# Kernel optimization log

Measured on AMD Instinct MI355X. Metric: run time of the kernel, lower is better.

The kernel has to match this reference:

```python
import jax, jax.numpy as jnp
import numpy as np

B, C, H, W = 32, 3, 224, 224
HID, EM, NCLS = 128, 64, 10


def _mlp(x, w1, b1, w2, b2):
    return jax.nn.relu(x @ w1 + b1) @ w2 + b2


def _grid(h, w):
    # generate_grid_coords(h, w, (-10,10), (-10,10)) -> [h*w, 2], row-major over (y, x)
    ys = jnp.linspace(-10.0, 10.0, h)
    xs = jnp.linspace(-10.0, 10.0, w)
    gy, gx = jnp.meshgrid(ys, xs, indexing='ij')
    return jnp.stack([gy.ravel(), gx.ravel()], axis=-1)


def setup_inputs() -> dict:
    key = jax.random.key(0)
    ks = jax.random.split(key, 16)
    def lin(k, fi, fo):
        return (jax.random.normal(k, (fi, fo), jnp.float32) / np.sqrt(fi)).astype(jnp.float32)
    inp = {"images": jax.random.normal(ks[0], (B, C, H, W), dtype=jnp.float32)}
    specs = [("obs", C, EM), ("loc", 2, EM), ("ol", 2 * EM, EM), ("cls", EM, NCLS)]
    i = 1
    for n, fi, fo in specs:
        inp[f"w_{n}1"] = lin(ks[i], fi, HID); i += 1
        inp[f"b_{n}1"] = jnp.zeros((HID,), jnp.float32)
        inp[f"w_{n}2"] = lin(ks[i], HID, fo); i += 1
        inp[f"b_{n}2"] = jnp.zeros((fo,), jnp.float32)
    return inp


def reference(images, w_obs1, b_obs1, w_obs2, b_obs2,
              w_loc1, b_loc1, w_loc2, b_loc2,
              w_ol1, b_ol1, w_ol2, b_ol2,
              w_cls1, b_cls1, w_cls2, b_cls2):
    b, c, h, w = images.shape
    n = h * w
    # to_set_representation: [B,C,H,W] -> [B, N, C]
    obss = images.reshape(b, c, n).transpose(0, 2, 1)
    locs = _grid(h, w)                                       # [N, 2]
    em_loc = _mlp(locs, w_loc1, b_loc1, w_loc2, b_loc2)       # [N, EM] (shared, tiled over batch)
    em_obs = _mlp(obss, w_obs1, b_obs1, w_obs2, b_obs2)       # [B, N, EM]
    em = jnp.concatenate(
        [em_obs, jnp.broadcast_to(em_loc[None], (b, n, em_loc.shape[-1]))], axis=-1)
    em_obsloc = _mlp(em, w_ol1, b_ol1, w_ol2, b_ol2)          # [B, N, EM]
    em_obsloc = jax.nn.softplus(em_obsloc)                    # non_negative=True
    em_set = em_obsloc.sum(axis=1)                            # sum-pool over set dim
    logits = _mlp(em_set, w_cls1, b_cls1, w_cls2, b_cls2)     # [B, NCLS]
    return logits
```

## Files before the change

kernel.cpp:

```cpp
#include <hip/hip_runtime.h>

#define N_PIX 50176
#define W_IMG 224
#define ROWS 32
#define NBX 24

typedef __attribute__((ext_vector_type(8))) short s8v;
typedef __attribute__((ext_vector_type(4))) float f4v;
typedef __attribute__((ext_vector_type(2))) __bf16 bf2v;

__device__ __forceinline__ unsigned short f2bf(float f) {
    __bf16 h = (__bf16)f;
    return __builtin_bit_cast(unsigned short, h);
}
__device__ __forceinline__ unsigned int pack2bf(float lo, float hi) {
    bf2v v = {(__bf16)lo, (__bf16)hi};
    return __builtin_bit_cast(unsigned int, v);
}

#define SWZ(r, cb)  (((r) << 8) + ((cb) ^ (((r) & 15) << 4)))
#define CSWZ(r, cb) (((r) << 7) + ((cb) ^ (((r) & 7) << 4)))

__device__ __forceinline__ void gld_lds16(const void* g, void* l) {
    __builtin_amdgcn_global_load_lds(
        (const __attribute__((address_space(1))) unsigned int*)g,
        (__attribute__((address_space(3))) unsigned int*)l, 16, 0, 0);
}

__global__ void k0_weights(const float* __restrict__ w_obs2, const float* __restrict__ b_obs2,
                           const float* __restrict__ w_ol1, const float* __restrict__ b_ol1,
                           const float* __restrict__ w_ol2, const float* __restrict__ w_loc2,
                           unsigned short* __restrict__ Wk,
                           unsigned short* __restrict__ wol2t,
                           unsigned short* __restrict__ wloc2t,
                           float* __restrict__ bias_c) {
    int bid = blockIdx.x, t = threadIdx.x;
    if (bid < 64) {
        int lin = bid * 256 + t;
        int n = lin >> 7, k = lin & 127;
        float s = 0.f;
        #pragma unroll
        for (int e = 0; e < 64; ++e) s = fmaf(w_obs2[k * 64 + e], w_ol1[e * 128 + n], s);
        Wk[n * 192 + k] = f2bf(s);
    } else if (bid < 96) {
        int lin = (bid - 64) * 256 + t;
        int n = lin >> 6, k = lin & 63;
        Wk[n * 192 + 128 + k] = f2bf(w_ol1[(64 + k) * 128 + n]);
    } else if (bid < 128) {
        int lin = (bid - 96) * 256 + t;
        int n = lin >> 7, k = lin & 127;
        wol2t[n * 128 + k] = f2bf(w_ol2[k * 64 + n]);
    } else if (bid < 160) {
        int lin = (bid - 128) * 256 + t;
        int n = lin >> 7, k = lin & 127;
        wloc2t[n * 128 + k] = f2bf(w_loc2[k * 64 + n]);
    } else {
        if (t < 128) {
            float s = b_ol1[t];
            #pragma unroll
            for (int e = 0; e < 64; ++e) s = fmaf(b_obs2[e], w_ol1[e * 128 + t], s);
            bias_c[t] = s;
        }
    }
}

__global__ __launch_bounds__(256) void k1_loc(
        const float* __restrict__ w_loc1, const float* __restrict__ b_loc1,
        const unsigned short* __restrict__ wloc2t, const float* __restrict__ b_loc2,
        unsigned short* __restrict__ emloc) {
    __shared__ char hbuf[64 * 256];
    typedef __attribute__((ext_vector_type(4))) unsigned int u4v;

    const int t = threadIdx.x;
    const int n0 = blockIdx.x * 64;
    const int row = t >> 2, h0 = (t & 3) * 32;
    {
        int n = n0 + row;
        int iy = n / W_IMG, ix = n % W_IMG;
        float y = -10.f + (20.f / 223.f) * (float)iy;
        float x = -10.f + (20.f / 223.f) * (float)ix;
        #pragma unroll
        for (int q4 = 0; q4 < 4; ++q4) {
            int hb = h0 + q4 * 8;
            u4v pk;
            #pragma unroll
            for (int jj = 0; jj < 2; ++jj) {
                f4v wy = *(const f4v*)(w_loc1 + hb + jj * 4);
                f4v wx = *(const f4v*)(w_loc1 + 128 + hb + jj * 4);
                f4v bb = *(const f4v*)(b_loc1 + hb + jj * 4);
                #pragma unroll
                for (int j2 = 0; j2 < 2; ++j2) {
                    float v0 = fmaxf(fmaf(y, wy[j2 * 2], fmaf(x, wx[j2 * 2], bb[j2 * 2])), 0.f);
                    float v1 = fmaxf(fmaf(y, wy[j2 * 2 + 1], fmaf(x, wx[j2 * 2 + 1], bb[j2 * 2 + 1])), 0.f);
                    pk[jj * 2 + j2] = pack2bf(v0, v1);
                }
            }
            *(u4v*)(hbuf + SWZ(row, hb * 2)) = pk;
        }
    }
    __syncthreads();
    {
        const int w = t >> 6, l = t & 63;
        const int l15 = l & 15, lg = l >> 4;
        s8v a[4];
        #pragma unroll
        for (int ks = 0; ks < 4; ++ks)
            a[ks] = *(const s8v*)(hbuf + SWZ(w * 16 + l15, ks * 64 + lg * 16));
        #pragma unroll
        for (int nt = 0; nt < 4; ++nt) {
            f4v acc = {0.f, 0.f, 0.f, 0.f};
            #pragma unroll
            for (int ks = 0; ks < 4; ++ks) {
                s8v bfr = *(const s8v*)(wloc2t + (nt * 16 + l15) * 128 + ks * 32 + lg * 8);
                acc = __builtin_amdgcn_mfma_f32_16x16x32_bf16(a[ks], bfr, acc, 0, 0, 0);
            }
            float bb = b_loc2[nt * 16 + l15];
            int o = nt * 16 + l15;
            #pragma unroll
            for (int r = 0; r < 4; ++r) {
                int n = n0 + w * 16 + lg * 4 + r;
                emloc[(size_t)n * 64 + (o ^ ((n & 7) << 3))] = f2bf(acc[r] + bb);
            }
        }
    }
}

__global__ __launch_bounds__(256, 2) void k2_main(
        const float* __restrict__ images,
        const float* __restrict__ w_obs1, const float* __restrict__ b_obs1,
        const unsigned short* __restrict__ Wk, const float* __restrict__ biasc,
        const unsigned short* __restrict__ wol2t, const float* __restrict__ b_ol2,
        const unsigned short* __restrict__ emloc,
        float* __restrict__ part)
{
    __shared__ char bufA[2][ROWS * 256];
    __shared__ char bufB[2][ROWS * 256];
    __shared__ char bufC[2][ROWS * 128];
    __shared__ f4v bufI4[2][24];
    __shared__ float red[4][16];

    const int t = threadIdx.x;
    const int w = t >> 6, l = t & 63;
    const int l15 = l & 15, lg = l >> 4;
    const int cq = w;
    const int bx = blockIdx.x, b = blockIdx.y;
    const int start = bx * 65 + (bx < 8 ? bx : 8);
    const int cnt = 65 + (bx < 8 ? 1 : 0);
    const size_t imgb = (size_t)b * 3 * N_PIX;
    #define PBASE(k) ((start + (k)) * ROWS)

    s8v a1[2];
    #pragma unroll
    for (int mt = 0; mt < 2; ++mt) {
        int hh = cq * 32 + mt * 16 + l15;
        unsigned int lo = pack2bf(w_obs1[hh], w_obs1[128 + hh]);
        unsigned int hi = pack2bf(w_obs1[256 + hh], b_obs1[hh]);
        if (lg != 0) { lo = 0u; hi = 0u; }
        typedef __attribute__((ext_vector_type(4))) unsigned int u4;
        u4 u = {lo, hi, 0u, 0u};
        a1[mt] = __builtin_bit_cast(s8v, u);
    }

    s8v bw[2][6];
    #pragma unroll
    for (int nt = 0; nt < 2; ++nt) {
        int col = cq * 32 + nt * 16 + l15;
        #pragma unroll
        for (int ks = 0; ks < 6; ++ks)
            bw[nt][ks] = *(const s8v*)(Wk + col * 192 + ks * 32 + lg * 8);
    }
    s8v w2f[4];
    {
        int o = cq * 16 + l15;
        #pragma unroll
        for (int ks = 0; ks < 4; ++ks)
            w2f[ks] = *(const s8v*)(wol2t + o * 128 + ks * 32 + lg * 8);
    }
    const f4v bias30 = *(const f4v*)(biasc + cq * 32 + lg * 4);
    const f4v bias31 = *(const f4v*)(biasc + cq * 32 + 16 + lg * 4);
    const f4v bias4  = *(const f4v*)(b_ol2 + cq * 16 + lg * 4);

    f4v spacc = {0.f, 0.f, 0.f, 0.f};

    if (w == 1 && l < 24) {
        const char* src = (const char*)(images + imgb + (l >> 3) * N_PIX + PBASE(0)) + (l & 7) * 16;
        gld_lds16(src, (char*)bufI4[0]);
    }
    __syncthreads();

    for (int i = 0; i <= cnt + 1; ++i) {
        const int par = i & 1;
        if (i < cnt) {
            const char* src = (const char*)emloc +
                (size_t)(PBASE(i) + w * 8 + (l >> 3)) * 128 + (l & 7) * 16;
            gld_lds16(src, (char*)bufC[par] + w * 1024);
        }
        if (i + 1 < cnt && w == 1 && l < 24) {
            const char* src = (const char*)(images + imgb + (l >> 3) * N_PIX +
                                            PBASE(i + 1)) + (l & 7) * 16;
            gld_lds16(src, (char*)bufI4[par ^ 1]);
        }
        if (i < cnt) {
            const float* bI = (const float*)bufI4[par];
            char* bA = bufA[par];
            #pragma unroll
            for (int nt2 = 0; nt2 < 2; ++nt2) {
                const int p = nt2 * 16 + l15;
                float x0 = bI[p], x1 = bI[32 + p], x2 = bI[64 + p];
                typedef __attribute__((ext_vector_type(4))) unsigned int u4;
                u4 u = {pack2bf(x0, x1), pack2bf(x2, 1.0f), 0u, 0u};
                s8v bfr = __builtin_bit_cast(s8v, u);
                #pragma unroll
                for (int mt = 0; mt < 2; ++mt) {
                    f4v acc = {0.f, 0.f, 0.f, 0.f};
                    acc = __builtin_amdgcn_mfma_f32_16x16x32_bf16(a1[mt], bfr, acc, 0, 0, 0);
                    f4v z = {0.f, 0.f, 0.f, 0.f};
                    acc = __builtin_elementwise_max(acc, z);
                    uint2 pk;
                    pk.x = pack2bf(acc[0], acc[1]);
                    pk.y = pack2bf(acc[2], acc[3]);
                    *(uint2*)(bA + SWZ(p, cq * 64 + mt * 32 + lg * 8)) = pk;
                }
            }
        }
        if (i >= 1 && i <= cnt) {
            const char* bA = bufA[par ^ 1];
            const char* bC = bufC[par ^ 1];
            char* bB = bufB[par ^ 1];
            #pragma unroll
            for (int ms = 0; ms < 2; ++ms) {
                const int p = ms * 16 + l15;
                s8v bf[4];
                #pragma unroll
                for (int ks = 0; ks < 4; ++ks)
                    bf[ks] = *(const s8v*)(bA + SWZ(p, ks * 64 + lg * 16));
                s8v c0 = *(const s8v*)(bC + CSWZ(p, lg * 16));
                s8v c1 = *(const s8v*)(bC + CSWZ(p, lg * 16 + 64));
                f4v acc0 = {0.f, 0.f, 0.f, 0.f}, acc1 = {0.f, 0.f, 0.f, 0.f};
                __builtin_amdgcn_s_setprio(1);
                #pragma unroll
                for (int ks = 0; ks < 4; ++ks) {
                    acc0 = __builtin_amdgcn_mfma_f32_16x16x32_bf16(bw[0][ks], bf[ks], acc0, 0, 0, 0);
                    acc1 = __builtin_amdgcn_mfma_f32_16x16x32_bf16(bw[1][ks], bf[ks], acc1, 0, 0, 0);
                }
                acc0 = __builtin_amdgcn_mfma_f32_16x16x32_bf16(bw[0][4], c0, acc0, 0, 0, 0);
                acc1 = __builtin_amdgcn_mfma_f32_16x16x32_bf16(bw[1][4], c0, acc1, 0, 0, 0);
                acc0 = __builtin_amdgcn_mfma_f32_16x16x32_bf16(bw[0][5], c1, acc0, 0, 0, 0);
                acc1 = __builtin_amdgcn_mfma_f32_16x16x32_bf16(bw[1][5], c1, acc1, 0, 0, 0);
                __builtin_amdgcn_s_setprio(0);
                f4v v0 = acc0 + bias30, v1 = acc1 + bias31;
                f4v z = {0.f, 0.f, 0.f, 0.f};
                v0 = __builtin_elementwise_max(v0, z);
                v1 = __builtin_elementwise_max(v1, z);
                uint2 w0p, w1p;
                w0p.x = pack2bf(v0[0], v0[1]);
                w0p.y = pack2bf(v0[2], v0[3]);
                w1p.x = pack2bf(v1[0], v1[1]);
                w1p.y = pack2bf(v1[2], v1[3]);
                *(uint2*)(bB + SWZ(p, cq * 64 + lg * 8)) = w0p;
                *(uint2*)(bB + SWZ(p, cq * 64 + 32 + lg * 8)) = w1p;
            }
        }
        if (i >= 2) {
            const char* bB = bufB[par];
            #pragma unroll
            for (int ms = 0; ms < 2; ++ms) {
                const int p = ms * 16 + l15;
                s8v bf[4];
                #pragma unroll
                for (int ks = 0; ks < 4; ++ks)
                    bf[ks] = *(const s8v*)(bB + SWZ(p, ks * 64 + lg * 16));
                f4v acc = {0.f, 0.f, 0.f, 0.f};
                __builtin_amdgcn_s_setprio(1);
                #pragma unroll
                for (int ks = 0; ks < 4; ++ks)
                    acc = __builtin_amdgcn_mfma_f32_16x16x32_bf16(w2f[ks], bf[ks], acc, 0, 0, 0);
                __builtin_amdgcn_s_setprio(0);
                #pragma unroll
                for (int r = 0; r < 4; ++r) {
                    float xv = acc[r] + bias4[r];
                    spacc[r] += fmaxf(xv, 0.f) + __logf(1.f + __expf(-fabsf(xv)));
                }
            }
        }
        __syncthreads();
    }

    #pragma unroll
    for (int m = 1; m <= 8; m <<= 1) {
        #pragma unroll
        for (int r = 0; r < 4; ++r) spacc[r] += __shfl_xor(spacc[r], m, 64);
    }
    if (l15 == 0) {
        #pragma unroll
        for (int r = 0; r < 4; ++r) red[w][lg * 4 + r] = spacc[r];
    }
    __syncthreads();
    if (t < 64) part[((size_t)b * NBX + bx) * 64 + t] = red[t >> 4][t & 15];
}

__global__ __launch_bounds__(128) void k3_cls(
        const float* __restrict__ part,
        const float* __restrict__ w_cls1, const float* __restrict__ b_cls1,
        const float* __restrict__ w_cls2, const float* __restrict__ b_cls2,
        float* __restrict__ out) {
    __shared__ float es[64];
    __shared__ float hid[128];
    const int b = blockIdx.x, t = threadIdx.x;
    if (t < 64) {
        float s = 0.f;
        #pragma unroll
        for (int x = 0; x < NBX; ++x) s += part[((size_t)b * NBX + x) * 64 + t];
        es[t] = s;
    }
    __syncthreads();
    {
        float s = b_cls1[t];
        #pragma unroll
        for (int e = 0; e < 64; ++e) s = fmaf(es[e], w_cls1[e * 128 + t], s);
        hid[t] = fmaxf(s, 0.f);
    }
    __syncthreads();
    if (t < 10) {
        float s = b_cls2[t];
        #pragma unroll
        for (int h = 0; h < 128; ++h) s = fmaf(hid[h], w_cls2[h * 10 + t], s);
        out[b * 10 + t] = s;
    }
}

extern "C" void kernel_launch(void* const* d_in, const int* in_sizes, int n_in,
                              void* d_out, int out_size, void* d_ws, size_t ws_size,
                              hipStream_t stream) {
    (void)in_sizes; (void)n_in; (void)out_size; (void)ws_size;
    const float* images = (const float*)d_in[0];
    const float* w_obs1 = (const float*)d_in[1];
    const float* b_obs1 = (const float*)d_in[2];
    const float* w_obs2 = (const float*)d_in[3];
    const float* b_obs2 = (const float*)d_in[4];
    const float* w_loc1 = (const float*)d_in[5];
    const float* b_loc1 = (const float*)d_in[6];
    const float* w_loc2 = (const float*)d_in[7];
    const float* b_loc2 = (const float*)d_in[8];
    const float* w_ol1  = (const float*)d_in[9];
    const float* b_ol1  = (const float*)d_in[10];
    const float* w_ol2  = (const float*)d_in[11];
    const float* b_ol2  = (const float*)d_in[12];
    const float* w_cls1 = (const float*)d_in[13];
    const float* b_cls1 = (const float*)d_in[14];
    const float* w_cls2 = (const float*)d_in[15];
    const float* b_cls2 = (const float*)d_in[16];

    char* ws = (char*)d_ws;
    float* part           = (float*)(ws);
    float* biasc          = (float*)(ws + 196608);
    unsigned short* Wk    = (unsigned short*)(ws + 197120);
    unsigned short* wol2t = (unsigned short*)(ws + 246272);
    unsigned short* wloc2t= (unsigned short*)(ws + 262656);
    unsigned short* emloc = (unsigned short*)(ws + 279040);

    hipLaunchKernelGGL(k0_weights, dim3(161), dim3(256), 0, stream,
                       w_obs2, b_obs2, w_ol1, b_ol1, w_ol2, w_loc2, Wk, wol2t, wloc2t, biasc);
    hipLaunchKernelGGL(k1_loc, dim3(784), dim3(256), 0, stream,
                       w_loc1, b_loc1, wloc2t, b_loc2, emloc);
    hipLaunchKernelGGL(k2_main, dim3(NBX, 32), dim3(256), 0, stream,
                       images, w_obs1, b_obs1, Wk, biasc, wol2t, b_ol2, emloc, part);
    hipLaunchKernelGGL(k3_cls, dim3(32), dim3(128), 0, stream,
                       part, w_cls1, b_cls1, w_cls2, b_cls2, (float*)d_out);
}
```

Measured before the change: 187.3 us.

## Switch stage-3 GEMM to 32x32x16 MFMA with bias-initialized accumulators

The obs-loc first-layer GEMM now uses one 32x32x16 bf16 MFMA tile per wave covering all 32 rows and 32 columns, replacing pairs of 16x16x32 MFMAs over two row sub-tiles. This halves the number of MFMA issues and cuts redundant LDS fragment reads. Biases are folded into the accumulator initial values instead of being added after, and softplus is rewritten with exp2/log2 to avoid extra scaling. The cost is higher register pressure from the 16-wide accumulator and 12 weight fragments, which may matter under launch_bounds(256,2).

```diff
diff --git a/kernel.cpp b/kernel.cpp
--- a/kernel.cpp
+++ b/kernel.cpp
@@ -7,6 +7,7 @@
 
 typedef __attribute__((ext_vector_type(8))) short s8v;
 typedef __attribute__((ext_vector_type(4))) float f4v;
+typedef __attribute__((ext_vector_type(16))) float f16v;
 typedef __attribute__((ext_vector_type(2))) __bf16 bf2v;
 
 __device__ __forceinline__ unsigned short f2bf(float f) {
@@ -143,6 +144,7 @@
     const int w = t >> 6, l = t & 63;
     const int l15 = l & 15, lg = l >> 4;
     const int cq = w;
+    const int l31 = l & 31, lh = l >> 5;
     const int bx = blockIdx.x, b = blockIdx.y;
     const int start = bx * 65 + (bx < 8 ? bx : 8);
     const int cnt = 65 + (bx < 8 ? 1 : 0);
@@ -161,14 +163,18 @@
         a1[mt] = __builtin_bit_cast(s8v, u);
     }
 
-    s8v bw[2][6];
+    s8v wk32[12];
+    {
+        const unsigned short* wr = Wk + (cq * 32 + l31) * 192 + lh * 8;
+        #pragma unroll
+        for (int ks = 0; ks < 12; ++ks)
+            wk32[ks] = *(const s8v*)(wr + ks * 16);
+    }
+    f4v bias16[4];
     #pragma unroll
-    for (int nt = 0; nt < 2; ++nt) {
-        int col = cq * 32 + nt * 16 + l15;
-        #pragma unroll
-        for (int ks = 0; ks < 6; ++ks)
-            bw[nt][ks] = *(const s8v*)(Wk + col * 192 + ks * 32 + lg * 8);
-    }
+    for (int q = 0; q < 4; ++q)
+        bias16[q] = *(const f4v*)(biasc + cq * 32 + 8 * q + 4 * lh);
+
     s8v w2f[4];
     {
         int o = cq * 16 + l15;
@@ -176,9 +182,7 @@
         for (int ks = 0; ks < 4; ++ks)
             w2f[ks] = *(const s8v*)(wol2t + o * 128 + ks * 32 + lg * 8);
     }
-    const f4v bias30 = *(const f4v*)(biasc + cq * 32 + lg * 4);
-    const f4v bias31 = *(const f4v*)(biasc + cq * 32 + 16 + lg * 4);
-    const f4v bias4  = *(const f4v*)(b_ol2 + cq * 16 + lg * 4);
+    const f4v bias4 = *(const f4v*)(b_ol2 + cq * 16 + lg * 4);
 
     f4v spacc = {0.f, 0.f, 0.f, 0.f};
 
@@ -227,50 +231,47 @@
             const char* bA = bufA[par ^ 1];
             const char* bC = bufC[par ^ 1];
             char* bB = bufB[par ^ 1];
+            f16v acc;
+            #pragma unroll
+            for (int q = 0; q < 4; ++q) {
+                acc[4 * q + 0] = bias16[q][0];
+                acc[4 * q + 1] = bias16[q][1];
+                acc[4 * q + 2] = bias16[q][2];
+                acc[4 * q + 3] = bias16[q][3];
+            }
+            __builtin_amdgcn_s_setprio(1);
+            #pragma unroll
+            for (int ks = 0; ks < 8; ++ks) {
+                s8v bfr = *(const s8v*)(bA + SWZ(l31, ks * 32 + lh * 16));
+                acc = __builtin_amdgcn_mfma_f32_32x32x16_bf16(wk32[ks], bfr, acc, 0, 0, 0);
+            }
+            #pragma unroll
+            for (int ks = 0; ks < 4; ++ks) {
+                s8v bfr = *(const s8v*)(bC + CSWZ(l31, ks * 32 + lh * 16));
+                acc = __builtin_amdgcn_mfma_f32_32x32x16_bf16(wk32[8 + ks], bfr, acc, 0, 0, 0);
+            }
+            __builtin_amdgcn_s_setprio(0);
+            #pragma unroll
+            for (int q = 0; q < 4; ++q) {
+                f4v v = {acc[4 * q], acc[4 * q + 1], acc[4 * q + 2], acc[4 * q + 3]};
+                f4v z = {0.f, 0.f, 0.f, 0.f};
+                v = __builtin_elementwise_max(v, z);
+                uint2 pk;
+                pk.x = pack2bf(v[0], v[1]);
+                pk.y = pack2bf(v[2], v[3]);
+                *(uint2*)(bB + SWZ(l31, cq * 64 + 16 * q + 8 * lh)) = pk;
+            }
+        }
+        if (i >= 2) {
+            const char* bB = bufB[par];
             #pragma unroll
             for (int ms = 0; ms < 2; ++ms) {
                 const int p = ms * 16 + l15;
                 s8v bf[4];
                 #pragma unroll
                 for (int ks = 0; ks < 4; ++ks)
-                    bf[ks] = *(const s8v*)(bA + SWZ(p, ks * 64 + lg * 16));
-                s8v c0 = *(const s8v*)(bC + CSWZ(p, lg * 16));
-                s8v c1 = *(const s8v*)(bC + CSWZ(p, lg * 16 + 64));
-                f4v acc0 = {0.f, 0.f, 0.f, 0.f}, acc1 = {0.f, 0.f, 0.f, 0.f};
-                __builtin_amdgcn_s_setprio(1);
-                #pragma unroll
-                for (int ks = 0; ks < 4; ++ks) {
-                    acc0 = __builtin_amdgcn_mfma_f32_16x16x32_bf16(bw[0][ks], bf[ks], acc0, 0, 0, 0);
-                    acc1 = __builtin_amdgcn_mfma_f32_16x16x32_bf16(bw[1][ks], bf[ks], acc1, 0, 0, 0);
-                }
-                acc0 = __builtin_amdgcn_mfma_f32_16x16x32_bf16(bw[0][4], c0, acc0, 0, 0, 0);
-                acc1 = __builtin_amdgcn_mfma_f32_16x16x32_bf16(bw[1][4], c0, acc1, 0, 0, 0);
-                acc0 = __builtin_amdgcn_mfma_f32_16x16x32_bf16(bw[0][5], c1, acc0, 0, 0, 0);
-                acc1 = __builtin_amdgcn_mfma_f32_16x16x32_bf16(bw[1][5], c1, acc1, 0, 0, 0);
-                __builtin_amdgcn_s_setprio(0);
-                f4v v0 = acc0 + bias30, v1 = acc1 + bias31;
-                f4v z = {0.f, 0.f, 0.f, 0.f};
-                v0 = __builtin_elementwise_max(v0, z);
-                v1 = __builtin_elementwise_max(v1, z);
-                uint2 w0p, w1p;
-                w0p.x = pack2bf(v0[0], v0[1]);
-                w0p.y = pack2bf(v0[2], v0[3]);
-                w1p.x = pack2bf(v1[0], v1[1]);
-                w1p.y = pack2bf(v1[2], v1[3]);
-                *(uint2*)(bB + SWZ(p, cq * 64 + lg * 8)) = w0p;
-                *(uint2*)(bB + SWZ(p, cq * 64 + 32 + lg * 8)) = w1p;
-            }
-        }
-        if (i >= 2) {
-            const char* bB = bufB[par];
-            #pragma unroll
-            for (int ms = 0; ms < 2; ++ms) {
-                const int p = ms * 16 + l15;
-                s8v bf[4];
-                #pragma unroll
-                for (int ks = 0; ks < 4; ++ks)
                     bf[ks] = *(const s8v*)(bB + SWZ(p, ks * 64 + lg * 16));
-                f4v acc = {0.f, 0.f, 0.f, 0.f};
+                f4v acc = bias4;
                 __builtin_amdgcn_s_setprio(1);
                 #pragma unroll
                 for (int ks = 0; ks < 4; ++ks)
@@ -278,8 +279,9 @@
                 __builtin_amdgcn_s_setprio(0);
                 #pragma unroll
                 for (int r = 0; r < 4; ++r) {
-                    float xv = acc[r] + bias4[r];
-                    spacc[r] += fmaxf(xv, 0.f) + __logf(1.f + __expf(-fabsf(xv)));
+                    float xv = acc[r];
+                    float e = exp2f(-1.44269504f * fabsf(xv));
+                    spacc[r] += fmaf(0.69314718f, log2f(1.f + e), fmaxf(xv, 0.f));
                 }
             }
         }
```

New measurement: 212.7 us. 1.14x slower.
